# Kernel optimization log

Measured on AMD Instinct MI355X. Metric: run time of the kernel, lower is better.

The kernel has to match this reference:

```python
import jax, jax.numpy as jnp
import numpy as np

D_MODEL = 1024
NUM_HEADS = 16
HEAD_DIM = D_MODEL // NUM_HEADS


def setup_inputs() -> dict:
    key = jax.random.key(0)
    ks = jax.random.split(key, 5)
    B, T = 4, 2048
    x = jax.random.normal(ks[0], (B, T, D_MODEL), dtype=jnp.float32)
    s = 1.0 / np.sqrt(D_MODEL)
    w_qkv = jax.random.normal(ks[1], (D_MODEL, 3 * D_MODEL), dtype=jnp.float32) * s
    b_qkv = jnp.zeros((3 * D_MODEL,), dtype=jnp.float32)
    w_out = jax.random.normal(ks[2], (D_MODEL, D_MODEL), dtype=jnp.float32) * s
    b_out = jnp.zeros((D_MODEL,), dtype=jnp.float32)
    return {"x": x, "w_qkv": w_qkv, "b_qkv": b_qkv, "w_out": w_out, "b_out": b_out}


def reference(x, w_qkv, b_qkv, w_out, b_out):
    B, T, C = x.shape
    H, Dh = NUM_HEADS, HEAD_DIM
    qkv = x @ w_qkv + b_qkv                      # [B,T,3C]
    qkv = qkv.reshape(B, T, 3, H, Dh)
    q = qkv[:, :, 0].transpose(0, 2, 1, 3)      # [B,H,T,Dh]
    k = qkv[:, :, 1].transpose(0, 2, 1, 3)
    v = qkv[:, :, 2].transpose(0, 2, 1, 3)
    scale = 1.0 / np.sqrt(Dh)
    attn = jnp.einsum('bhqd,bhkd->bhqk', q, k) * scale  # [B,H,T,T]
    causal = jnp.tril(jnp.ones((T, T), dtype=bool))
    attn = jnp.where(causal[None, None], attn, -jnp.inf)
    attn = jax.nn.softmax(attn, axis=-1)
    out = jnp.einsum('bhqk,bhkd->bhqd', attn, v)        # [B,H,T,Dh]
    out = out.transpose(0, 2, 1, 3).reshape(B, T, C)
    return out @ w_out + b_out
```

## Files before the change

### kernel.cpp

```cpp
#include <hip/hip_runtime.h>
#include <stdint.h>

typedef unsigned short u16;
typedef __attribute__((ext_vector_type(8))) __bf16 bf16x8;
typedef __attribute__((ext_vector_type(4))) float f32x4;
typedef __attribute__((ext_vector_type(4))) u16 u16x4;
typedef __attribute__((ext_vector_type(4))) uint32_t u32x4;

__device__ __forceinline__ u16 f2bf(float f) {
    union { float f; uint32_t u; } v; v.f = f;
    uint32_t r = (v.u + 0x7fffu + ((v.u >> 16) & 1u)) >> 16;
    return (u16)r;
}

__device__ __forceinline__ void gll16(const u16* g, u16* l) {
    __builtin_amdgcn_global_load_lds((const __attribute__((address_space(1))) uint32_t*)g,
                                     (__attribute__((address_space(3))) uint32_t*)l, 16, 0, 0);
}

__global__ void cast_kernel(const float* __restrict__ in, u16* __restrict__ out, int n) {
    int i = (blockIdx.x * blockDim.x + threadIdx.x) * 4;
    if (i + 3 < n) {
        float4 v = *(const float4*)(in + i);
        u16x4 o;
        o.x = f2bf(v.x); o.y = f2bf(v.y); o.z = f2bf(v.z); o.w = f2bf(v.w);
        *(u16x4*)(out + i) = o;
    }
}

__global__ void transpose_cast(const float* __restrict__ in, u16* __restrict__ out, int R, int C) {
    __shared__ float tile[32][33];
    int c0 = blockIdx.x * 32;
    int r0 = blockIdx.y * 32;
    int tx = threadIdx.x, ty = threadIdx.y;
#pragma unroll
    for (int i = 0; i < 32; i += 8)
        tile[ty + i][tx] = in[(size_t)(r0 + ty + i) * C + c0 + tx];
    __syncthreads();
#pragma unroll
    for (int i = 0; i < 32; i += 8)
        out[(size_t)(c0 + ty + i) * R + r0 + tx] = f2bf(tile[tx][ty + i]);
}

template <int EPI>
__global__ __launch_bounds__(256) void gemm_bt(
    const u16* __restrict__ A, const u16* __restrict__ Bt,
    int K, int N, const float* __restrict__ bias,
    u16* __restrict__ Qb, u16* __restrict__ Kb, u16* __restrict__ Vtb,
    float* __restrict__ Cout)
{
    __shared__ __align__(16) u16 As[128 * 32];
    __shared__ __align__(16) u16 Bs[128 * 32];
    __shared__ __align__(16) u16 vtr[EPI == 0 ? 4 * 64 * 72 : 4];

    const int tid  = threadIdx.x;
    const int lane = tid & 63;
    const int wave = tid >> 6;
    const int wm = (wave >> 1) * 64;
    const int wn = (wave & 1) * 64;
    const int l15 = lane & 15;
    const int l4  = lane >> 4;
    const int bm = blockIdx.x * 128;
    const int bn = blockIdx.y * 128;

    f32x4 acc[4][4];
#pragma unroll
    for (int i = 0; i < 4; i++)
#pragma unroll
        for (int j = 0; j < 4; j++)
            acc[i][j] = (f32x4){0.f, 0.f, 0.f, 0.f};

    const int r0 = tid >> 2;
    const int cc = (tid & 3) * 8;
    const u16* Ap = A + (size_t)(bm + r0) * K + cc;
    const u16* Bp = Bt + (size_t)(bn + r0) * K + cc;
    u16* AsW = As + wave * 512;
    u16* BsW = Bs + wave * 512;

    for (int k0 = 0; k0 < K; k0 += 32) {
        __syncthreads();
        gll16(Ap + k0, AsW);
        gll16(Ap + (size_t)64 * K + k0, AsW + 2048);
        gll16(Bp + k0, BsW);
        gll16(Bp + (size_t)64 * K + k0, BsW + 2048);
        __syncthreads();

        bf16x8 af[4];
#pragma unroll
        for (int mi = 0; mi < 4; mi++)
            af[mi] = *(const bf16x8*)&As[(wm + mi * 16 + l15) * 32 + l4 * 8];
#pragma unroll
        for (int ni = 0; ni < 4; ni++) {
            bf16x8 bf = *(const bf16x8*)&Bs[(wn + ni * 16 + l15) * 32 + l4 * 8];
#pragma unroll
            for (int mi = 0; mi < 4; mi++)
                acc[mi][ni] = __builtin_amdgcn_mfma_f32_16x16x32_bf16(af[mi], bf, acc[mi][ni], 0, 0, 0);
        }
    }

    if (EPI == 0 && blockIdx.y >= 16) {
        u16* tr = vtr + wave * (64 * 72);
#pragma unroll
        for (int mi = 0; mi < 4; mi++)
#pragma unroll
            for (int ni = 0; ni < 4; ni++)
#pragma unroll
                for (int r = 0; r < 4; r++) {
                    int d  = ni * 16 + l15;
                    int tl = mi * 16 + l4 * 4 + r;
                    int gn = bn + wn + ni * 16 + l15;
                    tr[d * 72 + tl] = f2bf(acc[mi][ni][r] + bias[gn]);
                }
        __syncthreads();
        const int hh = (bn + wn - 2048) >> 6;
        const int bb = (bm + wm) >> 11;
        const int tglob0 = (bm + wm) & 2047;
        const int t0 = (lane & 7) * 8;
#pragma unroll
        for (int it = 0; it < 8; it++) {
            int d = it * 8 + (lane >> 3);
            uint4 v = *(const uint4*)&tr[d * 72 + t0];
            *(uint4*)(Vtb + (((size_t)(bb * 16 + hh)) * 64 + d) * 2048 + tglob0 + t0) = v;
        }
        return;
    }

#pragma unroll
    for (int mi = 0; mi < 4; mi++) {
#pragma unroll
        for (int ni = 0; ni < 4; ni++) {
#pragma unroll
            for (int r = 0; r < 4; r++) {
                int gm = bm + wm + mi * 16 + l4 * 4 + r;
                int gn = bn + wn + ni * 16 + l15;
                float v = acc[mi][ni][r] + bias[gn];
                if (EPI == 0) {
                    int s = gn >> 10, rem = gn & 1023;
                    int h = rem >> 6, d = rem & 63;
                    int b = gm >> 11, t = gm & 2047;
                    size_t qkidx = (((size_t)(b * 16 + h)) * 2048 + t) * 64 + d;
                    if (s == 0)      Qb[qkidx] = f2bf(v * 0.125f);
                    else             Kb[qkidx] = f2bf(v);
                } else {
                    Cout[(size_t)gm * N + gn] = v;
                }
            }
        }
    }
}

__global__ __launch_bounds__(256) void attn_kernel(
    const u16* __restrict__ Qb, const u16* __restrict__ Kb,
    const u16* __restrict__ Vtb, u16* __restrict__ Ob)
{
    const int blk = blockIdx.x;
    const int qb  = 15 - (blk >> 6);
    const int bh  = blk & 63;
    const int b   = bh >> 4;
    const int h   = bh & 15;
    const u16* Qh = Qb + ((size_t)bh) * 2048 * 64;
    const u16* Kh = Kb + ((size_t)bh) * 2048 * 64;
    const u16* Vh = Vtb + ((size_t)bh) * 64 * 2048;

    __shared__ __align__(16) u16 KsBuf[2][128 * 64];
    __shared__ __align__(16) u16 VsBuf[2][64 * 128];

    const int tid  = threadIdx.x;
    const int wave = tid >> 6;
    const int lane = tid & 63;
    const int l15 = lane & 15;
    const int l4  = lane >> 4;

    const int addr_a = (((l4 & 1) * 32) + l15) * 4;
    const int addr_b = addr_a + 64;
    const bool hi_t  = (l4 & 2) != 0;

    const bf16x8 ones = __builtin_bit_cast(bf16x8,
        (u32x4){0x3F803F80u, 0x3F803F80u, 0x3F803F80u, 0x3F803F80u});

    const int qrow0 = qb * 128 + wave * 32;

    auto stage = [&](int j, int pb) {
#pragma unroll
        for (int i = 0; i < 4; i++) {
            int lu = i * 256 + tid;
            int rK = lu >> 3, uK = (lu & 7) ^ (rK & 7);
            gll16(Kh + ((size_t)(j * 128 + rK)) * 64 + uK * 8,
                  &KsBuf[pb][(i * 256 + wave * 64) * 8]);
            int rV = lu >> 4, uV = (lu & 15) ^ (rV & 15);
            gll16(Vh + (size_t)rV * 2048 + j * 128 + uV * 8,
                  &VsBuf[pb][(i * 256 + wave * 64) * 8]);
        }
    };

    bf16x8 qf[2][2];
#pragma unroll
    for (int mi = 0; mi < 2; mi++)
#pragma unroll
        for (int kd = 0; kd < 2; kd++)
            qf[mi][kd] = *(const bf16x8*)(Qh + (size_t)(qrow0 + mi * 16 + l15) * 64 + kd * 32 + l4 * 8);

    f32x4 Ot[4][2];
#pragma unroll
    for (int md = 0; md < 4; md++)
#pragma unroll
        for (int mi = 0; mi < 2; mi++)
            Ot[md][mi] = (f32x4){0.f, 0.f, 0.f, 0.f};
    f32x4 L[2];
    L[0] = (f32x4){0.f, 0.f, 0.f, 0.f};
    L[1] = (f32x4){0.f, 0.f, 0.f, 0.f};

    stage(0, 0);
    __syncthreads();

    int p = 0;
    for (int j = 0; j <= qb; ++j) {
        if (j < qb) stage(j + 1, p ^ 1);

        const u16* Kc = KsBuf[p];
        const u16* Vc = VsBuf[p];
        const bool diag = (j == qb);

#pragma unroll
        for (int kk = 0; kk < 4; kk++) {
            uint32_t pk[2][2][2];
#pragma unroll
            for (int tt = 0; tt < 2; tt++) {
                const int t = kk * 2 + tt;
                const int rr = t * 16 + l15;
                f32x4 St[2];
                St[0] = (f32x4){0.f, 0.f, 0.f, 0.f};
                St[1] = (f32x4){0.f, 0.f, 0.f, 0.f};
#pragma unroll
                for (int kd = 0; kd < 2; kd++) {
                    bf16x8 kf = *(const bf16x8*)&Kc[((rr << 3) + ((kd * 4 + l4) ^ (rr & 7))) * 8];
                    St[0] = __builtin_amdgcn_mfma_f32_16x16x32_bf16(kf, qf[0][kd], St[0], 0, 0, 0);
                    St[1] = __builtin_amdgcn_mfma_f32_16x16x32_bf16(kf, qf[1][kd], St[1], 0, 0, 0);
                }
#pragma unroll
                for (int mi = 0; mi < 2; mi++) {
                    int qloc = wave * 32 + mi * 16 + l15;
                    float pr[4];
#pragma unroll
                    for (int r = 0; r < 4; r++) {
                        float s = St[mi][r];
                        if (diag) {
                            int kvloc = t * 16 + l4 * 4 + r;
                            if (kvloc > qloc) s = -__builtin_inff();
                        }
                        pr[r] = __expf(s);
                    }
                    union { float f; uint32_t u; } u0, u1, u2, u3;
                    u0.f = pr[0]; u1.f = pr[1]; u2.f = pr[2]; u3.f = pr[3];
                    pk[tt][mi][0] = __builtin_amdgcn_perm(u1.u, u0.u, 0x07060302u);
                    pk[tt][mi][1] = __builtin_amdgcn_perm(u3.u, u2.u, 0x07060302u);
                }
            }

            bf16x8 vtf[4];
#pragma unroll
            for (int md = 0; md < 4; md++) {
                const int rr = md * 16 + l15;
                vtf[md] = *(const bf16x8*)&Vc[((rr << 4) + ((kk * 4 + l4) ^ (rr & 15))) * 8];
            }
#pragma unroll
            for (int mi = 0; mi < 2; mi++) {
                uint32_t s0a = __builtin_amdgcn_ds_bpermute(addr_a, pk[0][mi][0]);
                uint32_t s0b = __builtin_amdgcn_ds_bpermute(addr_a, pk[1][mi][0]);
                uint32_t s1a = __builtin_amdgcn_ds_bpermute(addr_a, pk[0][mi][1]);
                uint32_t s1b = __builtin_amdgcn_ds_bpermute(addr_a, pk[1][mi][1]);
                uint32_t s2a = __builtin_amdgcn_ds_bpermute(addr_b, pk[0][mi][0]);
                uint32_t s2b = __builtin_amdgcn_ds_bpermute(addr_b, pk[1][mi][0]);
                uint32_t s3a = __builtin_amdgcn_ds_bpermute(addr_b, pk[0][mi][1]);
                uint32_t s3b = __builtin_amdgcn_ds_bpermute(addr_b, pk[1][mi][1]);
                u32x4 pt;
                pt.x = hi_t ? s0b : s0a;
                pt.y = hi_t ? s1b : s1a;
                pt.z = hi_t ? s2b : s2a;
                pt.w = hi_t ? s3b : s3a;
                bf16x8 ptf = __builtin_bit_cast(bf16x8, pt);
#pragma unroll
                for (int md = 0; md < 4; md++)
                    Ot[md][mi] = __builtin_amdgcn_mfma_f32_16x16x32_bf16(vtf[md], ptf, Ot[md][mi], 0, 0, 0);
                L[mi] = __builtin_amdgcn_mfma_f32_16x16x32_bf16(ones, ptf, L[mi], 0, 0, 0);
            }
        }

        __syncthreads();
        p ^= 1;
    }

#pragma unroll
    for (int mi = 0; mi < 2; mi++) {
        float inv = 1.0f / L[mi][0];
        int t = qrow0 + mi * 16 + l15;
#pragma unroll
        for (int md = 0; md < 4; md++) {
            u16x4 o;
            o.x = f2bf(Ot[md][mi][0] * inv);
            o.y = f2bf(Ot[md][mi][1] * inv);
            o.z = f2bf(Ot[md][mi][2] * inv);
            o.w = f2bf(Ot[md][mi][3] * inv);
            *(u16x4*)(Ob + ((size_t)(b * 2048 + t)) * 1024 + h * 64 + md * 16 + l4 * 4) = o;
        }
    }
}

extern "C" void kernel_launch(void* const* d_in, const int* in_sizes, int n_in,
                              void* d_out, int out_size, void* d_ws, size_t ws_size,
                              hipStream_t stream) {
    const float* x     = (const float*)d_in[0];
    const float* w_qkv = (const float*)d_in[1];
    const float* b_qkv = (const float*)d_in[2];
    const float* w_out = (const float*)d_in[3];
    const float* b_out = (const float*)d_in[4];
    float* out = (float*)d_out;

    size_t off = 0;
    char* ws = (char*)d_ws;
    auto alloc = [&](size_t bytes) -> void* {
        void* p = ws + off;
        off += (bytes + 255) & ~(size_t)255;
        return p;
    };
    u16* xb    = (u16*)alloc((size_t)8192 * 1024 * 2);
    u16* wqkvT = (u16*)alloc((size_t)3072 * 1024 * 2);
    u16* woutT = (u16*)alloc((size_t)1024 * 1024 * 2);
    u16* Qb    = (u16*)alloc((size_t)8192 * 1024 * 2);
    u16* Kb    = (u16*)alloc((size_t)8192 * 1024 * 2);
    u16* Vtb   = (u16*)alloc((size_t)8192 * 1024 * 2);
    u16* Ob    = xb;

    cast_kernel<<<dim3(8192), dim3(256), 0, stream>>>(x, xb, 8192 * 1024);
    transpose_cast<<<dim3(3072 / 32, 1024 / 32), dim3(32, 8), 0, stream>>>(w_qkv, wqkvT, 1024, 3072);
    transpose_cast<<<dim3(1024 / 32, 1024 / 32), dim3(32, 8), 0, stream>>>(w_out, woutT, 1024, 1024);

    gemm_bt<0><<<dim3(64, 24), dim3(256), 0, stream>>>(xb, wqkvT, 1024, 3072, b_qkv, Qb, Kb, Vtb, nullptr);
    attn_kernel<<<dim3(1024), dim3(256), 0, stream>>>(Qb, Kb, Vtb, Ob);
    gemm_bt<1><<<dim3(64, 8), dim3(256), 0, stream>>>(Ob, woutT, 1024, 1024, b_out, nullptr, nullptr, nullptr, out);
}
```

Before: 270.8 us.

## Double-buffer GEMM LDS tiles and XOR-swizzle to avoid bank conflicts

The GEMM main loop now uses two LDS buffers and issues the global-to-LDS loads for the next K step before computing on the current one. This overlaps load latency with MFMA work and drops one barrier per iteration. Global source columns are XOR-swizzled by row and the LDS reads apply the matching swizzle, which is meant to cut bank conflicts on the fragment loads. The separate A, B and transpose arrays are merged into one shared buffer that the V-transpose epilogue reuses. This doubles the tile storage, but total LDS use changes little because of that reuse.

```diff
diff --git a/kernel.cpp b/kernel.cpp
--- a/kernel.cpp
+++ b/kernel.cpp
@@ -49,9 +49,7 @@
     u16* __restrict__ Qb, u16* __restrict__ Kb, u16* __restrict__ Vtb,
     float* __restrict__ Cout)
 {
-    __shared__ __align__(16) u16 As[128 * 32];
-    __shared__ __align__(16) u16 Bs[128 * 32];
-    __shared__ __align__(16) u16 vtr[EPI == 0 ? 4 * 64 * 72 : 4];
+    __shared__ __align__(16) u16 smem[EPI == 0 ? 18432 : 16384];
 
     const int tid  = threadIdx.x;
     const int lane = tid & 63;
@@ -71,35 +69,47 @@
             acc[i][j] = (f32x4){0.f, 0.f, 0.f, 0.f};
 
     const int r0 = tid >> 2;
-    const int cc = (tid & 3) * 8;
-    const u16* Ap = A + (size_t)(bm + r0) * K + cc;
-    const u16* Bp = Bt + (size_t)(bn + r0) * K + cc;
-    u16* AsW = As + wave * 512;
-    u16* BsW = Bs + wave * 512;
-
+    const int u0 = (tid & 3) ^ ((r0 >> 1) & 3);
+    const u16* Ap = A + (size_t)(bm + r0) * K + u0 * 8;
+    const u16* Bp = Bt + (size_t)(bn + r0) * K + u0 * 8;
+    const int su = (l15 >> 1) & 3;
+
+    auto stage = [&](int k0, int pb) {
+        u16* dst = smem + pb * 8192 + wave * 512;
+        gll16(Ap + k0, dst);
+        gll16(Ap + (size_t)64 * K + k0, dst + 2048);
+        gll16(Bp + k0, dst + 4096);
+        gll16(Bp + (size_t)64 * K + k0, dst + 6144);
+    };
+
+    stage(0, 0);
+    __syncthreads();
+
+    int p = 0;
     for (int k0 = 0; k0 < K; k0 += 32) {
-        __syncthreads();
-        gll16(Ap + k0, AsW);
-        gll16(Ap + (size_t)64 * K + k0, AsW + 2048);
-        gll16(Bp + k0, BsW);
-        gll16(Bp + (size_t)64 * K + k0, BsW + 2048);
-        __syncthreads();
+        if (k0 + 32 < K) stage(k0 + 32, p ^ 1);
+
+        const u16* AsP = smem + p * 8192;
+        const u16* BsP = AsP + 4096;
 
         bf16x8 af[4];
 #pragma unroll
         for (int mi = 0; mi < 4; mi++)
-            af[mi] = *(const bf16x8*)&As[(wm + mi * 16 + l15) * 32 + l4 * 8];
+            af[mi] = *(const bf16x8*)&AsP[(wm + mi * 16 + l15) * 32 + ((l4 ^ su) * 8)];
 #pragma unroll
         for (int ni = 0; ni < 4; ni++) {
-            bf16x8 bf = *(const bf16x8*)&Bs[(wn + ni * 16 + l15) * 32 + l4 * 8];
+            bf16x8 bf = *(const bf16x8*)&BsP[(wn + ni * 16 + l15) * 32 + ((l4 ^ su) * 8)];
 #pragma unroll
             for (int mi = 0; mi < 4; mi++)
                 acc[mi][ni] = __builtin_amdgcn_mfma_f32_16x16x32_bf16(af[mi], bf, acc[mi][ni], 0, 0, 0);
         }
+
+        __syncthreads();
+        p ^= 1;
     }
 
     if (EPI == 0 && blockIdx.y >= 16) {
-        u16* tr = vtr + wave * (64 * 72);
+        u16* tr = smem + wave * (64 * 72);
 #pragma unroll
         for (int mi = 0; mi < 4; mi++)
 #pragma unroll
```

After: 249.1 us. 1.09x faster.
